# Kernel optimization log

Measured on AMD Instinct MI355X. Metric: run time of the kernel, lower is better.

## Reference

```python
import jax, jax.numpy as jnp
import numpy as np

N_NODES = 50000
N_EDGES = 600000
IN_DIM = 128
HID_DIM = 128
OUT_DIM = 128
N_GRAPHS = 64


def _glorot(key, shape):
    lim = np.sqrt(6.0 / (shape[0] + shape[1]))
    return jax.random.uniform(key, shape, jnp.float32, -lim, lim)


def setup_inputs() -> dict:
    key = jax.random.key(0)
    ks = jax.random.split(key, 8)
    h = jax.random.normal(ks[0], (N_NODES, IN_DIM), jnp.float32)
    src = jax.random.randint(ks[1], (N_EDGES,), 0, N_NODES, jnp.int64)
    dst = jax.random.randint(ks[2], (N_EDGES,), 0, N_NODES, jnp.int64)
    graph_ids = jnp.sort(jax.random.randint(ks[3], (N_NODES,), 0, N_GRAPHS, jnp.int64))
    W1 = _glorot(ks[4], (IN_DIM, HID_DIM)); b1 = jnp.zeros((HID_DIM,), jnp.float32)
    W2 = _glorot(ks[5], (HID_DIM, HID_DIM)); b2 = jnp.zeros((HID_DIM,), jnp.float32)
    W3 = _glorot(ks[6], (HID_DIM, OUT_DIM)); b3 = jnp.zeros((OUT_DIM,), jnp.float32)
    return {"h": h, "src": src, "dst": dst, "graph_ids": graph_ids,
            "W1": W1, "b1": b1, "W2": W2, "b2": b2, "W3": W3, "b3": b3,
            "n_graphs": N_GRAPHS}


def _graph_conv(h, src, dst, norm_src, norm_dst, W, b):
    # DGL GraphConv, norm='both': D_dst^{-1/2} A^T D_src^{-1/2} h W + b
    m = h * norm_src[:, None]                                   # [N, d]
    agg = jax.ops.segment_sum(m[src], dst, num_segments=h.shape[0])  # [N, d]
    return (agg * norm_dst[:, None]) @ W + b


def reference(h, src, dst, graph_ids, W1, b1, W2, b2, W3, b3, n_graphs):
    n = h.shape[0]
    ones = jnp.ones((src.shape[0],), h.dtype)
    out_deg = jnp.clip(jax.ops.segment_sum(ones, src, num_segments=n), 1.0)
    in_deg = jnp.clip(jax.ops.segment_sum(ones, dst, num_segments=n), 1.0)
    norm_src = out_deg ** -0.5
    norm_dst = in_deg ** -0.5

    x = jax.nn.relu(_graph_conv(h, src, dst, norm_src, norm_dst, W1, b1))
    x = jax.nn.relu(_graph_conv(x, src, dst, norm_src, norm_dst, W2, b2))
    x = jax.nn.relu(_graph_conv(x, src, dst, norm_src, norm_dst, W3, b3))

    # dgl.mean_nodes: per-graph mean over nodes
    gsum = jax.ops.segment_sum(x, graph_ids, num_segments=n_graphs)          # [G, d]
    gcnt = jax.ops.segment_sum(jnp.ones((n,), x.dtype), graph_ids, num_segments=n_graphs)
    return gsum / jnp.clip(gcnt, 1.0)[:, None]
```

## Files before the change

kernel.cpp:

```cpp
#include <hip/hip_runtime.h>
#include <hip/hip_fp16.h>


#define DIM 128

typedef _Float16 half8 __attribute__((ext_vector_type(8)));
typedef float floatx4 __attribute__((ext_vector_type(4)));

#define HIST_R 4
#define HIST_S 64
#define NPR 12500
#define LDSW (NPR / 2)

__global__ __launch_bounds__(256) void k_hist(const int* __restrict__ src,
                                              const int* __restrict__ dst,
                                              unsigned* __restrict__ partial, int E) {
    __shared__ unsigned hist[LDSW];
    int b = blockIdx.x;
    int a = b / (HIST_R * HIST_S);
    int r = (b / HIST_S) % HIST_R;
    int s = b % HIST_S;
    const int* arr = a ? dst : src;
    for (int i = threadIdx.x; i < LDSW; i += 256) hist[i] = 0;
    __syncthreads();
    int chunk = (E + HIST_S - 1) / HIST_S;
    int e0 = s * chunk;
    int e1 = min(e0 + chunk, E);
    unsigned base = (unsigned)(r * NPR);
    for (int i = e0 + threadIdx.x; i < e1; i += 256) {
        unsigned n = (unsigned)arr[i] - base;
        if (n < NPR) atomicAdd(&hist[n >> 1], 1u << ((n & 1) * 16));
    }
    __syncthreads();
    unsigned* outp = partial + ((size_t)(a * HIST_R + r) * HIST_S + s) * LDSW;
    for (int i = threadIdx.x; i < LDSW; i += 256) outp[i] = hist[i];
}

__global__ void k_hist_merge(const unsigned* __restrict__ partial,
                             float* __restrict__ ns, float* __restrict__ nd,
                             int* __restrict__ inc, int N) {
    int t = blockIdx.x * blockDim.x + threadIdx.x;
    const int total_w = HIST_R * LDSW;
    if (t >= 2 * total_w) return;
    int a = t / total_w;
    int wg = t % total_w;
    int r = wg / LDSW;
    int w = wg % LDSW;
    const unsigned* p = partial + ((size_t)(a * HIST_R + r) * HIST_S) * LDSW + w;
    unsigned sum = 0;
#pragma unroll
    for (int s = 0; s < HIST_S; ++s) sum += p[(size_t)s * LDSW];
    int n0 = r * NPR + w * 2;
    int d0 = (int)(sum & 0xFFFFu);
    int d1 = (int)(sum >> 16);
    if (a == 0) {
        if (n0 < N)     ns[n0]     = rsqrtf(fmaxf((float)d0, 1.0f));
        if (n0 + 1 < N) ns[n0 + 1] = rsqrtf(fmaxf((float)d1, 1.0f));
    } else {
        if (n0 < N)     { nd[n0]     = rsqrtf(fmaxf((float)d0, 1.0f)); inc[n0]     = d0; }
        if (n0 + 1 < N) { nd[n0 + 1] = rsqrtf(fmaxf((float)d1, 1.0f)); inc[n0 + 1] = d1; }
    }
}

__global__ void k_scan_partial(const int* __restrict__ inc, int* __restrict__ bsum, int N) {
    __shared__ int s[256];
    int i = blockIdx.x * 256 + threadIdx.x;
    int t = threadIdx.x;
    s[t] = (i < N) ? inc[i] : 0;
    __syncthreads();
    for (int off = 128; off > 0; off >>= 1) {
        if (t < off) s[t] += s[t + off];
        __syncthreads();
    }
    if (t == 0) bsum[blockIdx.x] = s[0];
}

__global__ void k_scan_top(int* __restrict__ bsum, int nb) {
    __shared__ int s[256];
    int t = threadIdx.x;
    int v = (t < nb) ? bsum[t] : 0;
    s[t] = v;
    __syncthreads();
    for (int off = 1; off < 256; off <<= 1) {
        int u = (t >= off) ? s[t - off] : 0;
        __syncthreads();
        s[t] += u;
        __syncthreads();
    }
    if (t < nb) bsum[t] = s[t] - v;
}

__global__ void k_scan_write(const int* __restrict__ inc, const int* __restrict__ bsum,
                             int* __restrict__ row_ptr, int N) {
    __shared__ int s[256];
    int i = blockIdx.x * 256 + threadIdx.x;
    int t = threadIdx.x;
    int v = (i < N) ? inc[i] : 0;
    s[t] = v;
    __syncthreads();
    for (int off = 1; off < 256; off <<= 1) {
        int u = (t >= off) ? s[t - off] : 0;
        __syncthreads();
        s[t] += u;
        __syncthreads();
    }
    int ex = bsum[blockIdx.x] + s[t] - v;
    if (i < N) row_ptr[i] = ex;
    if (i == N - 1) row_ptr[N] = ex + v;
}

__global__ void k_cursor(const unsigned* __restrict__ partial, const int* __restrict__ row_ptr,
                         int* __restrict__ cur, int N) {
    int t = blockIdx.x * blockDim.x + threadIdx.x;
    if (t >= HIST_R * LDSW) return;
    int r = t / LDSW;
    int w = t % LDSW;
    int n0 = r * NPR + 2 * w;
    const unsigned* p = partial + ((size_t)(HIST_R + r) * HIST_S) * LDSW + w;
    int run0 = (n0 < N) ? row_ptr[n0] : 0;
    int run1 = (n0 + 1 < N) ? row_ptr[n0 + 1] : 0;
    int* c = cur + (size_t)r * HIST_S * NPR + 2 * w;
#pragma unroll
    for (int s = 0; s < HIST_S; ++s) {
        c[(size_t)s * NPR + 0] = run0;
        c[(size_t)s * NPR + 1] = run1;
        unsigned hv = p[(size_t)s * LDSW];
        run0 += (int)(hv & 0xFFFFu);
        run1 += (int)(hv >> 16);
    }
}

__global__ __launch_bounds__(256) void k_fill2(const int* __restrict__ src,
                                               const int* __restrict__ dst,
                                               const int* __restrict__ cur,
                                               int* __restrict__ csr, int E) {
    __shared__ int lcur[NPR];
    int r = blockIdx.x / HIST_S;
    int s = blockIdx.x % HIST_S;
    const int* cs = cur + (size_t)(r * HIST_S + s) * NPR;
    for (int i = threadIdx.x; i < NPR; i += 256) lcur[i] = cs[i];
    __syncthreads();
    int chunk = (E + HIST_S - 1) / HIST_S;
    int e0 = s * chunk;
    int e1 = min(e0 + chunk, E);
    unsigned base = (unsigned)(r * NPR);
    for (int i = e0 + threadIdx.x; i < e1; i += 256) {
        unsigned d = (unsigned)dst[i] - base;
        if (d < NPR) {
            int p = atomicAdd(&lcur[d], 1);
            csr[p] = src[i];
        }
    }
}

__global__ void k_h2half(const float4* __restrict__ h, const float* __restrict__ ns,
                         uint2* __restrict__ A, int N) {
    int i = blockIdx.x * blockDim.x + threadIdx.x;
    if (i < N * 32) {
        int n = i >> 5;
        float s = ns[n];
        float4 v = h[i];
        __half2 p0 = __floats2half2_rn(v.x * s, v.y * s);
        __half2 p1 = __floats2half2_rn(v.z * s, v.w * s);
        uint2 o;
        o.x = *(unsigned*)&p0;
        o.y = *(unsigned*)&p1;
        A[i] = o;
    }
}

__global__ void k_w2half3(const float* __restrict__ W1, const float* __restrict__ W2,
                          const float* __restrict__ W3, _Float16* __restrict__ Wt1,
                          _Float16* __restrict__ Wt2, _Float16* __restrict__ Wt3) {
    int i = blockIdx.x * blockDim.x + threadIdx.x;
    int j = i >> 14;
    int local = i & 16383;
    int k = local >> 7;
    int n = local & 127;
    const float* W = (j == 0) ? W1 : (j == 1) ? W2 : W3;
    _Float16* Wt = (j == 0) ? Wt1 : (j == 1) ? Wt2 : Wt3;
    Wt[(size_t)n * DIM + k] = (_Float16)W[local];
}

__global__ __launch_bounds__(256) void k_agg(const uint2* __restrict__ A,
                                             const int* __restrict__ row_ptr,
                                             const int* __restrict__ csr,
                                             const float* __restrict__ nd,
                                             uint2* __restrict__ Bh, int N) {
    int gtid = blockIdx.x * blockDim.x + threadIdx.x;
    int node = gtid >> 6;
    int lane = threadIdx.x & 63;
    if (node >= N) return;
    int e0 = row_ptr[node];
    int e1 = row_ptr[node + 1];
    int half = lane >> 5;
    int l8 = lane & 31;
    float ax = 0.f, ay = 0.f, az = 0.f, aw = 0.f;

    for (int base = e0; base < e1; base += 16) {
        int idx[8];
        uint2 u[8];
#pragma unroll
        for (int j = 0; j < 8; ++j) {
            int ee = base + 2 * j + half;
            idx[j] = csr[min(ee, e1 - 1)];
        }
#pragma unroll
        for (int j = 0; j < 8; ++j) {
            u[j] = A[(size_t)idx[j] * 32 + l8];
        }
#pragma unroll
        for (int j = 0; j < 8; ++j) {
            int ee = base + 2 * j + half;
            if (ee < e1) {
                __half2 p0 = *(__half2*)&u[j].x;
                __half2 p1 = *(__half2*)&u[j].y;
                float2 f0 = __half22float2(p0);
                float2 f1 = __half22float2(p1);
                ax += f0.x; ay += f0.y; az += f1.x; aw += f1.y;
            }
        }
    }

    ax += __shfl_xor(ax, 32);
    ay += __shfl_xor(ay, 32);
    az += __shfl_xor(az, 32);
    aw += __shfl_xor(aw, 32);

    if (half == 0) {
        float scale = nd[node];
        __half2 p0 = __floats2half2_rn(ax * scale, ay * scale);
        __half2 p1 = __floats2half2_rn(az * scale, aw * scale);
        uint2 o;
        o.x = *(unsigned*)&p0;
        o.y = *(unsigned*)&p1;
        Bh[(size_t)node * 32 + l8] = o;
    }
}

template <bool SCALE_NS>
__global__ __launch_bounds__(256) void k_gemm_mfma(
    const _Float16* __restrict__ Bin, const _Float16* __restrict__ Wt,
    const float* __restrict__ bias, const float* __restrict__ ns,
    _Float16* __restrict__ Xout, int N) {
    int tid = threadIdx.x;
    int wave = tid >> 6;
    int lane = tid & 63;
    int quad = lane >> 4;
    int l16 = lane & 15;
    int r0 = blockIdx.x * 64 + wave * 16;
    int arow = r0 + l16;

    half8 a[4];
#pragma unroll
    for (int q = 0; q < 4; ++q) {
        if (arow < N) {
            a[q] = *(const half8*)&Bin[(size_t)arow * DIM + q * 32 + quad * 8];
        } else {
            a[q] = half8{0, 0, 0, 0, 0, 0, 0, 0};
        }
    }

    floatx4 acc[8];
#pragma unroll
    for (int c = 0; c < 8; ++c) acc[c] = floatx4{0.f, 0.f, 0.f, 0.f};

#pragma unroll
    for (int c = 0; c < 8; ++c) {
#pragma unroll
        for (int q = 0; q < 4; ++q) {
            half8 b = *(const half8*)&Wt[(size_t)(c * 16 + l16) * DIM + q * 32 + quad * 8];
            acc[c] = __builtin_amdgcn_mfma_f32_16x16x32_f16(a[q], b, acc[c], 0, 0, 0);
        }
    }

    float bb[8];
#pragma unroll
    for (int c = 0; c < 8; ++c) bb[c] = bias[c * 16 + l16];

#pragma unroll
    for (int r = 0; r < 4; ++r) {
        int row = r0 + quad * 4 + r;
        if (row >= N) continue;
        float sr = SCALE_NS ? ns[row] : 1.0f;
#pragma unroll
        for (int c = 0; c < 8; ++c) {
            float v = fmaxf(acc[c][r] + bb[c], 0.0f);
            Xout[(size_t)row * DIM + c * 16 + l16] = (_Float16)(v * sr);
        }
    }
}

#define POOL_NODES 32
__global__ void k_pool_partial(const _Float16* __restrict__ X, const int* __restrict__ gid,
                               float* __restrict__ gsum, int* __restrict__ gcnt, int N) {
    int n0 = blockIdx.x * POOL_NODES;
    int d = threadIdx.x;
    int nend = min(n0 + POOL_NODES, N);
    float run = 0.0f;
    int cnt = 0;
    int curg = -1;
    for (int n = n0; n < nend; ++n) {
        int g = gid[n];
        if (g != curg) {
            if (cnt > 0) {
                atomicAdd(&gsum[curg * DIM + d], run);
                if (d == 0) atomicAdd(&gcnt[curg], cnt);
            }
            run = 0.0f; cnt = 0; curg = g;
        }
        run += (float)X[(size_t)n * DIM + d];
        cnt++;
    }
    if (cnt > 0) {
        atomicAdd(&gsum[curg * DIM + d], run);
        if (d == 0) atomicAdd(&gcnt[curg], cnt);
    }
}

__global__ void k_finalize(const float* __restrict__ gsum, const int* __restrict__ gcnt,
                           float* __restrict__ out, int G) {
    int i = blockIdx.x * blockDim.x + threadIdx.x;
    if (i < G * DIM) {
        int g = i >> 7;
        float c = fmaxf((float)gcnt[g], 1.0f);
        out[i] = gsum[i] / c;
    }
}

extern "C" void kernel_launch(void* const* d_in, const int* in_sizes, int n_in,
                              void* d_out, int out_size, void* d_ws, size_t ws_size,
                              hipStream_t stream) {
    const float* h   = (const float*)d_in[0];
    const int*   src = (const int*)d_in[1];
    const int*   dst = (const int*)d_in[2];
    const int*   gid = (const int*)d_in[3];
    const float* W1  = (const float*)d_in[4];
    const float* b1  = (const float*)d_in[5];
    const float* W2  = (const float*)d_in[6];
    const float* b2  = (const float*)d_in[7];
    const float* W3  = (const float*)d_in[8];
    const float* b3  = (const float*)d_in[9];

    const int N = in_sizes[0] / DIM;
    const int E = in_sizes[1];
    const int G = 64;
    float* out = (float*)d_out;

    char* ws = (char*)d_ws;
    size_t off = 0;
    auto alloc = [&](size_t bytes) -> void* {
        void* p = ws + off;
        off += (bytes + 255) & ~(size_t)255;
        return p;
    };
    const int scanBlocks = (N + 255) / 256;
    uint2* Ah0     = (uint2*)alloc((size_t)N * DIM * 2);
    uint2* Ah1     = (uint2*)alloc((size_t)N * DIM * 2);
    uint2* Bh      = (uint2*)alloc((size_t)N * DIM * 2);
    _Float16* X3   = (_Float16*)alloc((size_t)N * DIM * 2);
    _Float16* Wt1  = (_Float16*)alloc((size_t)DIM * DIM * 2);
    _Float16* Wt2  = (_Float16*)alloc((size_t)DIM * DIM * 2);
    _Float16* Wt3  = (_Float16*)alloc((size_t)DIM * DIM * 2);
    float* ns      = (float*)alloc((size_t)N * 4);
    float* nd      = (float*)alloc((size_t)N * 4);
    int*   inc     = (int*)alloc((size_t)N * 4);
    unsigned* partial = (unsigned*)alloc((size_t)2 * HIST_R * HIST_S * LDSW * 4);
    int*   cur     = (int*)alloc((size_t)HIST_R * HIST_S * NPR * 4);
    int*   row_ptr = (int*)alloc((size_t)(N + 1) * 4);
    int*   csr     = (int*)alloc((size_t)E * 4);
    float* gsum    = (float*)alloc((size_t)G * DIM * 4);
    int*   gcnt    = (int*)alloc((size_t)G * 4);
    int*   bsum    = (int*)alloc((size_t)scanBlocks * 4);

    hipMemsetAsync(gsum, 0, (size_t)G * DIM * 4, stream);
    hipMemsetAsync(gcnt, 0, (size_t)G * 4, stream);

    k_hist<<<2 * HIST_R * HIST_S, 256, 0, stream>>>(src, dst, partial, E);
    int mergeThreads = 2 * HIST_R * LDSW;
    k_hist_merge<<<(mergeThreads + 255) / 256, 256, 0, stream>>>(partial, ns, nd, inc, N);

    k_scan_partial<<<scanBlocks, 256, 0, stream>>>(inc, bsum, N);
    k_scan_top<<<1, 256, 0, stream>>>(bsum, scanBlocks);
    k_scan_write<<<scanBlocks, 256, 0, stream>>>(inc, bsum, row_ptr, N);

    int curThreads = HIST_R * LDSW;
    k_cursor<<<(curThreads + 255) / 256, 256, 0, stream>>>(partial, row_ptr, cur, N);
    k_fill2<<<HIST_R * HIST_S, 256, 0, stream>>>(src, dst, cur, csr, E);

    k_w2half3<<<192, 256, 0, stream>>>(W1, W2, W3, Wt1, Wt2, Wt3);

    int aggBlocks  = (N * 64 + 255) / 256;
    int gemmBlocks = (N + 63) / 64;

    k_h2half<<<(N * 32 + 255) / 256, 256, 0, stream>>>((const float4*)h, ns, Ah0, N);
    k_agg<<<aggBlocks, 256, 0, stream>>>(Ah0, row_ptr, csr, nd, Bh, N);
    k_gemm_mfma<true><<<gemmBlocks, 256, 0, stream>>>((const _Float16*)Bh, Wt1, b1, ns, (_Float16*)Ah1, N);
    k_agg<<<aggBlocks, 256, 0, stream>>>(Ah1, row_ptr, csr, nd, Bh, N);
    k_gemm_mfma<true><<<gemmBlocks, 256, 0, stream>>>((const _Float16*)Bh, Wt2, b2, ns, (_Float16*)Ah0, N);
    k_agg<<<aggBlocks, 256, 0, stream>>>(Ah0, row_ptr, csr, nd, Bh, N);
    k_gemm_mfma<false><<<gemmBlocks, 256, 0, stream>>>((const _Float16*)Bh, Wt3, b3, ns, X3, N);

    k_pool_partial<<<(N + POOL_NODES - 1) / POOL_NODES, 128, 0, stream>>>(X3, gid, gsum, gcnt, N);
    k_finalize<<<(G * DIM + 255) / 256, 256, 0, stream>>>(gsum, gcnt, out, G);
}
```

Before: 317.8 us.

## Partition aggregation gathers by source range and fuse small prep kernels

The neighbour gather in k_agg now makes four passes over each node's edge list. Each pass only loads source rows whose index falls in one quarter of the node range, and issues those loads in groups of four. The aim is to keep concurrent gathers inside a smaller slice of the feature matrix for better cache locality. The cost is reading the CSR list four times, divergent branches between the two half-waves, and fewer independent loads in flight per thread. Separately, the gsum/gcnt memsets are folded into k_cursor and the weight conversion is merged into the h-to-half kernel, which cuts launch overhead.

```diff
diff --git a/kernel.cpp b/kernel.cpp
--- a/kernel.cpp
+++ b/kernel.cpp
@@ -3,6 +3,8 @@
 
 
 #define DIM 128
+#define GRAPHS 64
+#define RANGES 4
 
 typedef _Float16 half8 __attribute__((ext_vector_type(8)));
 typedef float floatx4 __attribute__((ext_vector_type(4)));
@@ -110,8 +112,11 @@
 }
 
 __global__ void k_cursor(const unsigned* __restrict__ partial, const int* __restrict__ row_ptr,
-                         int* __restrict__ cur, int N) {
+                         int* __restrict__ cur, float* __restrict__ gsum,
+                         int* __restrict__ gcnt, int N) {
     int t = blockIdx.x * blockDim.x + threadIdx.x;
+    if (t < GRAPHS * DIM) gsum[t] = 0.0f;
+    if (t < GRAPHS) gcnt[t] = 0;
     if (t >= HIST_R * LDSW) return;
     int r = t / LDSW;
     int w = t % LDSW;
@@ -153,10 +158,14 @@
     }
 }
 
-__global__ void k_h2half(const float4* __restrict__ h, const float* __restrict__ ns,
-                         uint2* __restrict__ A, int N) {
+__global__ void k_prep(const float4* __restrict__ h, const float* __restrict__ ns,
+                       uint2* __restrict__ A,
+                       const float* __restrict__ W1, const float* __restrict__ W2,
+                       const float* __restrict__ W3, _Float16* __restrict__ Wt1,
+                       _Float16* __restrict__ Wt2, _Float16* __restrict__ Wt3, int N) {
     int i = blockIdx.x * blockDim.x + threadIdx.x;
-    if (i < N * 32) {
+    int nf4 = N * 32;
+    if (i < nf4) {
         int n = i >> 5;
         float s = ns[n];
         float4 v = h[i];
@@ -166,20 +175,18 @@
         o.x = *(unsigned*)&p0;
         o.y = *(unsigned*)&p1;
         A[i] = o;
-    }
-}
-
-__global__ void k_w2half3(const float* __restrict__ W1, const float* __restrict__ W2,
-                          const float* __restrict__ W3, _Float16* __restrict__ Wt1,
-                          _Float16* __restrict__ Wt2, _Float16* __restrict__ Wt3) {
-    int i = blockIdx.x * blockDim.x + threadIdx.x;
-    int j = i >> 14;
-    int local = i & 16383;
-    int k = local >> 7;
-    int n = local & 127;
-    const float* W = (j == 0) ? W1 : (j == 1) ? W2 : W3;
-    _Float16* Wt = (j == 0) ? Wt1 : (j == 1) ? Wt2 : Wt3;
-    Wt[(size_t)n * DIM + k] = (_Float16)W[local];
+    } else {
+        int j = i - nf4;
+        if (j < 3 * 16384) {
+            int which = j >> 14;
+            int local = j & 16383;
+            int k = local >> 7;
+            int n = local & 127;
+            const float* W = (which == 0) ? W1 : (which == 1) ? W2 : W3;
+            _Float16* Wt = (which == 0) ? Wt1 : (which == 1) ? Wt2 : Wt3;
+            Wt[(size_t)n * DIM + k] = (_Float16)W[local];
+        }
+    }
 }
 
 __global__ __launch_bounds__(256) void k_agg(const uint2* __restrict__ A,
@@ -197,29 +204,36 @@
     int l8 = lane & 31;
     float ax = 0.f, ay = 0.f, az = 0.f, aw = 0.f;
 
-    for (int base = e0; base < e1; base += 16) {
-        int idx[8];
-        uint2 u[8];
-#pragma unroll
-        for (int j = 0; j < 8; ++j) {
-            int ee = base + 2 * j + half;
-            idx[j] = csr[min(ee, e1 - 1)];
-        }
-#pragma unroll
-        for (int j = 0; j < 8; ++j) {
-            u[j] = A[(size_t)idx[j] * 32 + l8];
-        }
-#pragma unroll
-        for (int j = 0; j < 8; ++j) {
-            int ee = base + 2 * j + half;
-            if (ee < e1) {
-                __half2 p0 = *(__half2*)&u[j].x;
-                __half2 p1 = *(__half2*)&u[j].y;
-                float2 f0 = __half22float2(p0);
-                float2 f1 = __half22float2(p1);
-                ax += f0.x; ay += f0.y; az += f1.x; aw += f1.y;
+    auto acc4 = [&](uint2 u) {
+        __half2 p0 = *(__half2*)&u.x;
+        __half2 p1 = *(__half2*)&u.y;
+        float2 f0 = __half22float2(p0);
+        float2 f1 = __half22float2(p1);
+        ax += f0.x; ay += f0.y; az += f1.x; aw += f1.y;
+    };
+
+#pragma unroll 1
+    for (int r = 0; r < RANGES; ++r) {
+        unsigned lo = (unsigned)(r * NPR);
+        int b0 = 0, b1 = 0, b2 = 0, b3 = 0;
+        int nb = 0;
+        for (int e = e0 + half; e < e1; e += 2) {
+            int idx = csr[e];
+            if ((unsigned)idx - lo < NPR) {
+                b0 = b1; b1 = b2; b2 = b3; b3 = idx;
+                if (++nb == 4) {
+                    uint2 u0 = A[(size_t)b0 * 32 + l8];
+                    uint2 u1 = A[(size_t)b1 * 32 + l8];
+                    uint2 u2 = A[(size_t)b2 * 32 + l8];
+                    uint2 u3 = A[(size_t)b3 * 32 + l8];
+                    acc4(u0); acc4(u1); acc4(u2); acc4(u3);
+                    nb = 0;
+                }
             }
         }
+        if (nb > 0) acc4(A[(size_t)b3 * 32 + l8]);
+        if (nb > 1) acc4(A[(size_t)b2 * 32 + l8]);
+        if (nb > 2) acc4(A[(size_t)b1 * 32 + l8]);
     }
 
     ax += __shfl_xor(ax, 32);
@@ -344,7 +358,7 @@
 
     const int N = in_sizes[0] / DIM;
     const int E = in_sizes[1];
-    const int G = 64;
+    const int G = GRAPHS;
     float* out = (float*)d_out;
 
     char* ws = (char*)d_ws;
@@ -373,9 +387,6 @@
     int*   gcnt    = (int*)alloc((size_t)G * 4);
     int*   bsum    = (int*)alloc((size_t)scanBlocks * 4);
 
-    hipMemsetAsync(gsum, 0, (size_t)G * DIM * 4, stream);
-    hipMemsetAsync(gcnt, 0, (size_t)G * 4, stream);
-
     k_hist<<<2 * HIST_R * HIST_S, 256, 0, stream>>>(src, dst, partial, E);
     int mergeThreads = 2 * HIST_R * LDSW;
     k_hist_merge<<<(mergeThreads + 255) / 256, 256, 0, stream>>>(partial, ns, nd, inc, N);
@@ -385,15 +396,16 @@
     k_scan_write<<<scanBlocks, 256, 0, stream>>>(inc, bsum, row_ptr, N);
 
     int curThreads = HIST_R * LDSW;
-    k_cursor<<<(curThreads + 255) / 256, 256, 0, stream>>>(partial, row_ptr, cur, N);
+    k_cursor<<<(curThreads + 255) / 256, 256, 0, stream>>>(partial, row_ptr, cur, gsum, gcnt, N);
     k_fill2<<<HIST_R * HIST_S, 256, 0, stream>>>(src, dst, cur, csr, E);
 
-    k_w2half3<<<192, 256, 0, stream>>>(W1, W2, W3, Wt1, Wt2, Wt3);
+    int prepThreads = N * 32 + 3 * 16384;
+    k_prep<<<(prepThreads + 255) / 256, 256, 0, stream>>>((const float4*)h, ns, Ah0,
+                                                          W1, W2, W3, Wt1, Wt2, Wt3, N);
 
     int aggBlocks  = (N * 64 + 255) / 256;
     int gemmBlocks = (N + 63) / 64;
 
-    k_h2half<<<(N * 32 + 255) / 256, 256, 0, stream>>>((const float4*)h, ns, Ah0, N);
     k_agg<<<aggBlocks, 256, 0, stream>>>(Ah0, row_ptr, csr, nd, Bh, N);
     k_gemm_mfma<true><<<gemmBlocks, 256, 0, stream>>>((const _Float16*)Bh, Wt1, b1, ns, (_Float16*)Ah1, N);
     k_agg<<<aggBlocks, 256, 0, stream>>>(Ah1, row_ptr, csr, nd, Bh, N);
```

Measured after the change: 499.3 us. 57.1% more time.

## Fuse CSR build and prep kernels to cut launch count

Applied to the files above, without the earlier changes.

Merges the degree merge with the block-sum reduction, folds the cursor computation and the zeroing of pool accumulators into the scan-write kernel, and combines the feature and weight fp16 conversions into one prep kernel. This removes several kernel launches and two memsets, so less time goes to launch gaps in a preprocessing chain made of many tiny kernels. The merge kernel now reads the histogram per node rather than per node pair, which doubles its partial reads. The cursor writes now come from only half the threads of each scan block.

```diff
diff --git a/kernel.cpp b/kernel.cpp
--- a/kernel.cpp
+++ b/kernel.cpp
@@ -3,6 +3,7 @@
 
 
 #define DIM 128
+#define GRAPHS 64
 
 typedef _Float16 half8 __attribute__((ext_vector_type(8)));
 typedef float floatx4 __attribute__((ext_vector_type(4)));
@@ -36,43 +37,40 @@
     for (int i = threadIdx.x; i < LDSW; i += 256) outp[i] = hist[i];
 }
 
-__global__ void k_hist_merge(const unsigned* __restrict__ partial,
-                             float* __restrict__ ns, float* __restrict__ nd,
-                             int* __restrict__ inc, int N) {
-    int t = blockIdx.x * blockDim.x + threadIdx.x;
-    const int total_w = HIST_R * LDSW;
-    if (t >= 2 * total_w) return;
-    int a = t / total_w;
-    int wg = t % total_w;
-    int r = wg / LDSW;
-    int w = wg % LDSW;
-    const unsigned* p = partial + ((size_t)(a * HIST_R + r) * HIST_S) * LDSW + w;
-    unsigned sum = 0;
-#pragma unroll
-    for (int s = 0; s < HIST_S; ++s) sum += p[(size_t)s * LDSW];
-    int n0 = r * NPR + w * 2;
-    int d0 = (int)(sum & 0xFFFFu);
-    int d1 = (int)(sum >> 16);
-    if (a == 0) {
-        if (n0 < N)     ns[n0]     = rsqrtf(fmaxf((float)d0, 1.0f));
-        if (n0 + 1 < N) ns[n0 + 1] = rsqrtf(fmaxf((float)d1, 1.0f));
-    } else {
-        if (n0 < N)     { nd[n0]     = rsqrtf(fmaxf((float)d0, 1.0f)); inc[n0]     = d0; }
-        if (n0 + 1 < N) { nd[n0 + 1] = rsqrtf(fmaxf((float)d1, 1.0f)); inc[n0 + 1] = d1; }
-    }
-}
-
-__global__ void k_scan_partial(const int* __restrict__ inc, int* __restrict__ bsum, int N) {
-    __shared__ int s[256];
-    int i = blockIdx.x * 256 + threadIdx.x;
-    int t = threadIdx.x;
-    s[t] = (i < N) ? inc[i] : 0;
-    __syncthreads();
-    for (int off = 128; off > 0; off >>= 1) {
-        if (t < off) s[t] += s[t + off];
+__global__ __launch_bounds__(256) void k_hist_merge(const unsigned* __restrict__ partial,
+                                                    float* __restrict__ ns,
+                                                    float* __restrict__ nd,
+                                                    int* __restrict__ inc,
+                                                    int* __restrict__ bsum, int N) {
+    __shared__ int sred[256];
+    int nb = (N + 255) / 256;
+    int isDst = (blockIdx.x < nb) ? 1 : 0;
+    int cb = isDst ? blockIdx.x : blockIdx.x - nb;
+    int n = cb * 256 + threadIdx.x;
+    int deg = 0;
+    if (n < N) {
+        int a = isDst ? 1 : 0;
+        int r = n / NPR;
+        int w = (n % NPR) >> 1;
+        int field = (n & 1) * 16;
+        const unsigned* p = partial + ((size_t)(a * HIST_R + r) * HIST_S) * LDSW + w;
+        unsigned sum = 0;
+#pragma unroll
+        for (int s = 0; s < HIST_S; ++s) sum += p[(size_t)s * LDSW];
+        deg = (int)((sum >> field) & 0xFFFFu);
+        float nrm = rsqrtf(fmaxf((float)deg, 1.0f));
+        if (isDst) { nd[n] = nrm; inc[n] = deg; }
+        else       { ns[n] = nrm; }
+    }
+    if (isDst) {
+        sred[threadIdx.x] = deg;
         __syncthreads();
-    }
-    if (t == 0) bsum[blockIdx.x] = s[0];
+        for (int off = 128; off > 0; off >>= 1) {
+            if (threadIdx.x < off) sred[threadIdx.x] += sred[threadIdx.x + off];
+            __syncthreads();
+        }
+        if (threadIdx.x == 0) bsum[cb] = sred[0];
+    }
 }
 
 __global__ void k_scan_top(int* __restrict__ bsum, int nb) {
@@ -90,10 +88,17 @@
     if (t < nb) bsum[t] = s[t] - v;
 }
 
-__global__ void k_scan_write(const int* __restrict__ inc, const int* __restrict__ bsum,
-                             int* __restrict__ row_ptr, int N) {
+__global__ __launch_bounds__(256) void k_scan_write(const int* __restrict__ inc,
+                                                    const int* __restrict__ bsum,
+                                                    const unsigned* __restrict__ partial,
+                                                    int* __restrict__ row_ptr,
+                                                    int* __restrict__ cur,
+                                                    float* __restrict__ gsum,
+                                                    int* __restrict__ gcnt, int N) {
     __shared__ int s[256];
-    int i = blockIdx.x * 256 + threadIdx.x;
+    __shared__ int exs[256];
+    int B = blockIdx.x * 256;
+    int i = B + threadIdx.x;
     int t = threadIdx.x;
     int v = (i < N) ? inc[i] : 0;
     s[t] = v;
@@ -105,28 +110,33 @@
         __syncthreads();
     }
     int ex = bsum[blockIdx.x] + s[t] - v;
+    exs[t] = ex;
     if (i < N) row_ptr[i] = ex;
     if (i == N - 1) row_ptr[N] = ex + v;
-}
-
-__global__ void k_cursor(const unsigned* __restrict__ partial, const int* __restrict__ row_ptr,
-                         int* __restrict__ cur, int N) {
-    int t = blockIdx.x * blockDim.x + threadIdx.x;
-    if (t >= HIST_R * LDSW) return;
-    int r = t / LDSW;
-    int w = t % LDSW;
-    int n0 = r * NPR + 2 * w;
-    const unsigned* p = partial + ((size_t)(HIST_R + r) * HIST_S) * LDSW + w;
-    int run0 = (n0 < N) ? row_ptr[n0] : 0;
-    int run1 = (n0 + 1 < N) ? row_ptr[n0 + 1] : 0;
-    int* c = cur + (size_t)r * HIST_S * NPR + 2 * w;
-#pragma unroll
-    for (int s = 0; s < HIST_S; ++s) {
-        c[(size_t)s * NPR + 0] = run0;
-        c[(size_t)s * NPR + 1] = run1;
-        unsigned hv = p[(size_t)s * LDSW];
-        run0 += (int)(hv & 0xFFFFu);
-        run1 += (int)(hv >> 16);
+    if (blockIdx.x == 0) {
+        for (int j = t; j < GRAPHS * DIM; j += 256) gsum[j] = 0.0f;
+        if (t < GRAPHS) gcnt[t] = 0;
+    }
+    __syncthreads();
+
+    if (t < 128) {
+        int n0 = B + 2 * t;
+        if (n0 < N) {
+            int r = n0 / NPR;
+            int w = (n0 % NPR) >> 1;
+            const unsigned* p = partial + ((size_t)(HIST_R + r) * HIST_S) * LDSW + w;
+            int run0 = exs[2 * t];
+            int run1 = exs[2 * t + 1];
+            int* c = cur + (size_t)r * HIST_S * NPR + 2 * w;
+#pragma unroll
+            for (int sl = 0; sl < HIST_S; ++sl) {
+                c[(size_t)sl * NPR + 0] = run0;
+                c[(size_t)sl * NPR + 1] = run1;
+                unsigned hv = p[(size_t)sl * LDSW];
+                run0 += (int)(hv & 0xFFFFu);
+                run1 += (int)(hv >> 16);
+            }
+        }
     }
 }
 
@@ -153,10 +163,14 @@
     }
 }
 
-__global__ void k_h2half(const float4* __restrict__ h, const float* __restrict__ ns,
-                         uint2* __restrict__ A, int N) {
+__global__ void k_prep(const float4* __restrict__ h, const float* __restrict__ ns,
+                       uint2* __restrict__ A,
+                       const float* __restrict__ W1, const float* __restrict__ W2,
+                       const float* __restrict__ W3, _Float16* __restrict__ Wt1,
+                       _Float16* __restrict__ Wt2, _Float16* __restrict__ Wt3, int N) {
     int i = blockIdx.x * blockDim.x + threadIdx.x;
-    if (i < N * 32) {
+    int nf4 = N * 32;
+    if (i < nf4) {
         int n = i >> 5;
         float s = ns[n];
         float4 v = h[i];
@@ -166,20 +180,18 @@
         o.x = *(unsigned*)&p0;
         o.y = *(unsigned*)&p1;
         A[i] = o;
-    }
-}
-
-__global__ void k_w2half3(const float* __restrict__ W1, const float* __restrict__ W2,
-                          const float* __restrict__ W3, _Float16* __restrict__ Wt1,
-                          _Float16* __restrict__ Wt2, _Float16* __restrict__ Wt3) {
-    int i = blockIdx.x * blockDim.x + threadIdx.x;
-    int j = i >> 14;
-    int local = i & 16383;
-    int k = local >> 7;
-    int n = local & 127;
-    const float* W = (j == 0) ? W1 : (j == 1) ? W2 : W3;
-    _Float16* Wt = (j == 0) ? Wt1 : (j == 1) ? Wt2 : Wt3;
-    Wt[(size_t)n * DIM + k] = (_Float16)W[local];
+    } else {
+        int j = i - nf4;
+        if (j < 3 * 16384) {
+            int which = j >> 14;
+            int local = j & 16383;
+            int k = local >> 7;
+            int n = local & 127;
+            const float* W = (which == 0) ? W1 : (which == 1) ? W2 : W3;
+            _Float16* Wt = (which == 0) ? Wt1 : (which == 1) ? Wt2 : Wt3;
+            Wt[(size_t)n * DIM + k] = (_Float16)W[local];
+        }
+    }
 }
 
 __global__ __launch_bounds__(256) void k_agg(const uint2* __restrict__ A,
@@ -344,7 +356,7 @@
 
     const int N = in_sizes[0] / DIM;
     const int E = in_sizes[1];
-    const int G = 64;
+    const int G = GRAPHS;
     float* out = (float*)d_out;
 
     char* ws = (char*)d_ws;
@@ -354,7 +366,7 @@
         off += (bytes + 255) & ~(size_t)255;
         return p;
     };
-    const int scanBlocks = (N + 255) / 256;
+    const int nb = (N + 255) / 256;
     uint2* Ah0     = (uint2*)alloc((size_t)N * DIM * 2);
     uint2* Ah1     = (uint2*)alloc((size_t)N * DIM * 2);
     uint2* Bh      = (uint2*)alloc((size_t)N * DIM * 2);
@@ -371,29 +383,21 @@
     int*   csr     = (int*)alloc((size_t)E * 4);
     float* gsum    = (float*)alloc((size_t)G * DIM * 4);
     int*   gcnt    = (int*)alloc((size_t)G * 4);
-    int*   bsum    = (int*)alloc((size_t)scanBlocks * 4);
-
-    hipMemsetAsync(gsum, 0, (size_t)G * DIM * 4, stream);
-    hipMemsetAsync(gcnt, 0, (size_t)G * 4, stream);
+    int*   bsum    = (int*)alloc((size_t)nb * 4);
 
     k_hist<<<2 * HIST_R * HIST_S, 256, 0, stream>>>(src, dst, partial, E);
-    int mergeThreads = 2 * HIST_R * LDSW;
-    k_hist_merge<<<(mergeThreads + 255) / 256, 256, 0, stream>>>(partial, ns, nd, inc, N);
-
-    k_scan_partial<<<scanBlocks, 256, 0, stream>>>(inc, bsum, N);
-    k_scan_top<<<1, 256, 0, stream>>>(bsum, scanBlocks);
-    k_scan_write<<<scanBlocks, 256, 0, stream>>>(inc, bsum, row_ptr, N);
-
-    int curThreads = HIST_R * LDSW;
-    k_cursor<<<(curThreads + 255) / 256, 256, 0, stream>>>(partial, row_ptr, cur, N);
+    k_hist_merge<<<2 * nb, 256, 0, stream>>>(partial, ns, nd, inc, bsum, N);
+    k_scan_top<<<1, 256, 0, stream>>>(bsum, nb);
+    k_scan_write<<<nb, 256, 0, stream>>>(inc, bsum, partial, row_ptr, cur, gsum, gcnt, N);
     k_fill2<<<HIST_R * HIST_S, 256, 0, stream>>>(src, dst, cur, csr, E);
 
-    k_w2half3<<<192, 256, 0, stream>>>(W1, W2, W3, Wt1, Wt2, Wt3);
+    int prepThreads = N * 32 + 3 * 16384;
+    k_prep<<<(prepThreads + 255) / 256, 256, 0, stream>>>((const float4*)h, ns, Ah0,
+                                                          W1, W2, W3, Wt1, Wt2, Wt3, N);
 
     int aggBlocks  = (N * 64 + 255) / 256;
     int gemmBlocks = (N + 63) / 64;
 
-    k_h2half<<<(N * 32 + 255) / 256, 256, 0, stream>>>((const float4*)h, ns, Ah0, N);
     k_agg<<<aggBlocks, 256, 0, stream>>>(Ah0, row_ptr, csr, nd, Bh, N);
     k_gemm_mfma<true><<<gemmBlocks, 256, 0, stream>>>((const _Float16*)Bh, Wt1, b1, ns, (_Float16*)Ah1, N);
     k_agg<<<aggBlocks, 256, 0, stream>>>(Ah1, row_ptr, csr, nd, Bh, N);
```

Result: no change. 311.9 us (-1.8%).
